# Kernel optimization log

Hardware: AMD Instinct MI355X
Metric: run time of the kernel (lower is better)

Reference implementation:

```python
import jax, jax.numpy as jnp
import numpy as np

B, S, D, H = 2, 2048, 1024, 16
HD = D // H
SCALE = HD ** -0.5


def setup_inputs() -> dict:
    key = jax.random.key(0)
    ks = jax.random.split(key, 9)
    w = 0.02
    return {
        "query": jax.random.normal(ks[0], (B, S, D), jnp.float32),
        "key": jax.random.normal(ks[1], (B, S, D), jnp.float32),
        "value": jax.random.normal(ks[2], (B, S, D), jnp.float32),
        # precomputed structural bias matrix B_struct [B, S, S]
        "bias_struct": jax.random.uniform(ks[3], (B, S, S), jnp.float32, 0.0, 1.5),
        "Wq": jax.random.normal(ks[4], (D, D), jnp.float32) * w,
        "bq": jnp.zeros((D,), jnp.float32),
        "Wk": jax.random.normal(ks[5], (D, D), jnp.float32) * w,
        "bk": jnp.zeros((D,), jnp.float32),
        "Wv": jax.random.normal(ks[6], (D, D), jnp.float32) * w,
        "bv": jnp.zeros((D,), jnp.float32),
        "Wo": jax.random.normal(ks[7], (D, D), jnp.float32) * w,
        "bo": jnp.zeros((D,), jnp.float32),
        "lambda_bias": jnp.array(1.0, jnp.float32),
    }


def _split_heads(x):
    # [B, S, D] -> [B, H, S, HD]
    b, s, _ = x.shape
    return x.reshape(b, s, H, HD).transpose(0, 2, 1, 3)


def reference(query, key, value, bias_struct, Wq, bq, Wk, bk, Wv, bv, Wo, bo, lambda_bias):
    # Linear projections (torch Linear: x @ W.T + b)
    Q = _split_heads(query @ Wq.T + bq)
    K = _split_heads(key @ Wk.T + bk)
    V = _split_heads(value @ Wv.T + bv)
    # scores = QK^T * scale + lambda * B_struct (broadcast over heads)
    scores = jnp.einsum("bhqd,bhkd->bhqk", Q, K) * SCALE
    scores = scores + lambda_bias * bias_struct[:, None, :, :]
    attn = jax.nn.softmax(scores, axis=-1)
    out = jnp.einsum("bhqk,bhkd->bhqd", attn, V)
    out = out.transpose(0, 2, 1, 3).reshape(query.shape[0], query.shape[1], D)
    return out @ Wo.T + bo
```

## Files before the change

### kernel.cpp

```cpp
#include <hip/hip_runtime.h>
#include <hip/hip_bf16.h>

namespace {

constexpr int B  = 2;
constexpr int S  = 2048;
constexpr int D  = 1024;
constexpr int H  = 16;
constexpr int BH = B * H;
constexpr float SCALE = 0.125f;
constexpr float LOG2E = 1.44269504f;
constexpr float SL2   = SCALE * LOG2E;
constexpr float THR2  = 8.0f * LOG2E;

constexpr int GM = B * S;
constexpr int GN = D;
constexpr int GK = D;

typedef __bf16 bf16x8 __attribute__((ext_vector_type(8)));
typedef float  f32x4  __attribute__((ext_vector_type(4)));
typedef unsigned short u16;
typedef u16 u16x8 __attribute__((ext_vector_type(8)));
typedef u16 u16x4 __attribute__((ext_vector_type(4)));

__device__ __forceinline__ u16 f2bf(float f) {
  union { float f; unsigned u; } v{f};
  unsigned r = v.u + 0x7fffu + ((v.u >> 16) & 1u);
  return (u16)(r >> 16);
}
__device__ __forceinline__ float bf2f(u16 u) {
  union { unsigned u; float f; } v{(unsigned)u << 16};
  return v.f;
}

__device__ __forceinline__ f32x4 mfma16(bf16x8 a, bf16x8 b, f32x4 c) {
  return __builtin_amdgcn_mfma_f32_16x16x32_bf16(a, b, c, 0, 0, 0);
}

__device__ __forceinline__ void gload_lds16(const u16* g, u16* l) {
  __builtin_amdgcn_global_load_lds(
      (const __attribute__((address_space(1))) void*)g,
      (__attribute__((address_space(3))) void*)l, 16, 0, 0);
}

__global__ __launch_bounds__(256) void cvt3_k(
    const float* __restrict__ a, const float* __restrict__ b,
    const float* __restrict__ c, u16* __restrict__ da,
    u16* __restrict__ db, u16* __restrict__ dc)
{
  const float* s = (blockIdx.z == 0) ? a : (blockIdx.z == 1) ? b : c;
  u16* d = (blockIdx.z == 0) ? da : (blockIdx.z == 1) ? db : dc;
  size_t i = ((size_t)blockIdx.x * 256 + threadIdx.x) * 4;
  float4 v = *(const float4*)&s[i];
  u16x4 o = { f2bf(v.x), f2bf(v.y), f2bf(v.z), f2bf(v.w) };
  *(u16x4*)&d[i] = o;
}

__global__ __launch_bounds__(256) void cvt4_k(
    const float* __restrict__ a, const float* __restrict__ b,
    const float* __restrict__ c, const float* __restrict__ e,
    u16* __restrict__ da, u16* __restrict__ db,
    u16* __restrict__ dc, u16* __restrict__ de)
{
  const float* s = (blockIdx.z == 0) ? a : (blockIdx.z == 1) ? b
                 : (blockIdx.z == 2) ? c : e;
  u16* d = (blockIdx.z == 0) ? da : (blockIdx.z == 1) ? db
         : (blockIdx.z == 2) ? dc : de;
  size_t i = ((size_t)blockIdx.x * 256 + threadIdx.x) * 4;
  float4 v = *(const float4*)&s[i];
  u16x4 o = { f2bf(v.x), f2bf(v.y), f2bf(v.z), f2bf(v.w) };
  *(u16x4*)&d[i] = o;
}

template <bool OUTBF, int NZ>
__global__ __launch_bounds__(256) void gemm_k(
    const u16* __restrict__ A0, const u16* __restrict__ A1, const u16* __restrict__ A2,
    const u16* __restrict__ W0, const u16* __restrict__ W1, const u16* __restrict__ W2,
    const float* __restrict__ b0, const float* __restrict__ b1, const float* __restrict__ b2,
    u16* __restrict__ C0, u16* __restrict__ C1, u16* __restrict__ C2,
    float* __restrict__ Cf)
{
  constexpr int BM = 128, BN = 64, BK = 64;
  __shared__ u16 Al[2][BM * BK];
  __shared__ u16 Bl[2][BN * BK];

  const int z = (NZ > 1) ? blockIdx.z : 0;
  const u16* Ap = (z == 0) ? A0 : (z == 1) ? A1 : A2;
  const u16* Wp = (z == 0) ? W0 : (z == 1) ? W1 : W2;
  const float* bias = (z == 0) ? b0 : (z == 1) ? b1 : b2;
  u16* Cb = (z == 0) ? C0 : (z == 1) ? C1 : C2;

  const int tid  = threadIdx.x;
  const int lane = tid & 63;
  const int w    = tid >> 6;
  const int wr = w >> 1, wc = w & 1;
  const int lg = lane >> 4, ll = lane & 15;
  const int bm = blockIdx.y * BM, bn = blockIdx.x * BN;

  auto STAGE = [&](int buf, int k0) {
#pragma unroll
    for (int i = 0; i < 4; ++i) {
      const int c = i * 256 + tid;
      const int row = c >> 3, cs = c & 7;
      const int dofs = ((cs * 16) ^ ((row & 7) << 4)) >> 1;
      gload_lds16(&Ap[(size_t)(bm + row) * GK + k0 + dofs], &Al[buf][c * 8]);
    }
#pragma unroll
    for (int i = 0; i < 2; ++i) {
      const int c = i * 256 + tid;
      const int row = c >> 3, cs = c & 7;
      const int dofs = ((cs * 16) ^ ((row & 7) << 4)) >> 1;
      gload_lds16(&Wp[(size_t)(bn + row) * GK + k0 + dofs], &Bl[buf][c * 8]);
    }
  };

  f32x4 acc[4][2] = {};

  STAGE(0, 0);
  __syncthreads();

  int cur = 0;
  constexpr int NT = GK / BK;
  for (int t = 0; t < NT; ++t) {
    if (t + 1 < NT) STAGE(cur ^ 1, (t + 1) * BK);
#pragma unroll
    for (int half = 0; half < 2; ++half) {
      bf16x8 af[4], bfr[2];
#pragma unroll
      for (int mi = 0; mi < 4; ++mi) {
        const int row = wr * 64 + mi * 16 + ll;
        af[mi] = *(const bf16x8*)&Al[cur][row * 64 +
                   (((half * 64 + lg * 16) ^ ((row & 7) << 4)) >> 1)];
      }
#pragma unroll
      for (int ni = 0; ni < 2; ++ni) {
        const int row = wc * 32 + ni * 16 + ll;
        bfr[ni] = *(const bf16x8*)&Bl[cur][row * 64 +
                   (((half * 64 + lg * 16) ^ ((row & 7) << 4)) >> 1)];
      }
#pragma unroll
      for (int mi = 0; mi < 4; ++mi)
#pragma unroll
        for (int ni = 0; ni < 2; ++ni)
          acc[mi][ni] = mfma16(af[mi], bfr[ni], acc[mi][ni]);
    }
    __syncthreads();
    cur ^= 1;
  }

#pragma unroll
  for (int ni = 0; ni < 2; ++ni) {
    const int gcol = bn + wc * 32 + ni * 16 + ll;
    const float bv = bias[gcol];
#pragma unroll
    for (int mi = 0; mi < 4; ++mi) {
      const int grow = bm + wr * 64 + mi * 16 + lg * 4;
#pragma unroll
      for (int r = 0; r < 4; ++r) {
        float v = acc[mi][ni][r] + bv;
        if (OUTBF) Cb[(size_t)(grow + r) * GN + gcol] = f2bf(v);
        else       Cf[(size_t)(grow + r) * GN + gcol] = v;
      }
    }
  }
}

__global__ __launch_bounds__(256) void transpose_v_k(
    const u16* __restrict__ Vb, u16* __restrict__ Vt)
{
  __shared__ u16 T[64][72];
  const int tid = threadIdx.x;
  const int bh = blockIdx.y, b = bh >> 4, h = bh & 15;
  const int s0 = blockIdx.x * 64;
#pragma unroll
  for (int it = 0; it < 2; ++it) {
    int idx = tid + it * 256;
    int s = idx >> 3, dc = idx & 7;
    *(uint4*)&T[s][dc * 8] =
        *(const uint4*)&Vb[(size_t)(b * S + s0 + s) * D + h * 64 + dc * 8];
  }
  __syncthreads();
#pragma unroll
  for (int it = 0; it < 2; ++it) {
    int idx = tid + it * 256;
    int d = idx >> 3, sc = idx & 7;
    u16x8 o;
#pragma unroll
    for (int jj = 0; jj < 8; ++jj) o[jj] = T[sc * 8 + jj][d];
    *(u16x8*)&Vt[((size_t)bh * 64 + d) * S + s0 + sc * 8] = o;
  }
}

__global__ __launch_bounds__(256) void attn_split_k(
    const u16* __restrict__ Qb, const u16* __restrict__ Kb,
    const u16* __restrict__ Vt, const float* __restrict__ biasS,
    const float* __restrict__ lamp, u16* __restrict__ Opart,
    float2* __restrict__ Ml)
{
  __shared__ u16 Kl[2][64 * 64];
  __shared__ __bf16 Pl[4][16][72];

  const int tid  = threadIdx.x;
  const int lane = tid & 63;
  const int w    = tid >> 6;
  const int lg = lane >> 4, ll = lane & 15;
  const int bh = blockIdx.y, b = bh >> 4, h = bh & 15;
  const int qw = blockIdx.x * 64 + w * 16;
  const int split = blockIdx.z;
  const int kvbase = split * (S / 2);
  const float lamS = lamp[0] * 8.0f;

  bf16x8 aQ[2];
  {
    const u16* qrow = &Qb[(size_t)(b * S + qw + ll) * D + h * 64];
    aQ[0] = *(const bf16x8*)&qrow[lg * 8];
    aQ[1] = *(const bf16x8*)&qrow[32 + lg * 8];
  }

  const u16* Kbase = &Kb[(size_t)(b * S + kvbase) * D + h * 64];
  const u16* Vbase = &Vt[(size_t)bh * 64 * S + kvbase];
  const float* Bb  = &biasS[((size_t)b * S + qw + lg * 4) * S + kvbase];

  auto STAGE_K = [&](int buf, int k0) {
#pragma unroll
    for (int i = 0; i < 2; ++i) {
      const int c   = (w * 2 + i) * 64 + lane;
      const int row = c >> 3, cs = c & 7;
      const int dofs = ((cs * 16) ^ ((row & 7) << 4)) >> 1;
      gload_lds16(&Kbase[(size_t)(k0 + row) * D + dofs],
                  &Kl[buf][(w * 2 + i) * 512]);
    }
  };

  f32x4 accO[4] = {};
  float m_r[4], l_r[4];
#pragma unroll
  for (int r = 0; r < 4; ++r) { m_r[r] = -1e30f; l_r[r] = 0.f; }

  STAGE_K(0, 0);
  __syncthreads();

  int cur = 0;
  constexpr int NT = (S / 2) / 64;
  for (int t = 0; t < NT; ++t) {
    const int k0 = t * 64;
    if (t + 1 < NT) STAGE_K(cur ^ 1, k0 + 64);

    f32x4 sf[4];
#pragma unroll
    for (int kf = 0; kf < 4; ++kf) {
      const int row = kf * 16 + ll;
      const u16* kr = &Kl[cur][row * 64];
      bf16x8 kb0 = *(const bf16x8*)&kr[((lg * 16) ^ ((row & 7) << 4)) >> 1];
      bf16x8 kb1 = *(const bf16x8*)&kr[((64 + lg * 16) ^ ((row & 7) << 4)) >> 1];
      f32x4 t4;
#pragma unroll
      for (int r = 0; r < 4; ++r)
        t4[r] = lamS * Bb[(size_t)r * S + k0 + kf * 16 + ll];
      t4 = mfma16(aQ[0], kb0, t4);
      t4 = mfma16(aQ[1], kb1, t4);
#pragma unroll
      for (int r = 0; r < 4; ++r) t4[r] *= SL2;
      sf[kf] = t4;
    }

    float pm[4];
#pragma unroll
    for (int r = 0; r < 4; ++r)
      pm[r] = fmaxf(fmaxf(sf[0][r], sf[1][r]), fmaxf(sf[2][r], sf[3][r]));
    float ex = fmaxf(fmaxf(pm[0] - m_r[0], pm[1] - m_r[1]),
                     fmaxf(pm[2] - m_r[2], pm[3] - m_r[3]));
    if (__any(ex > THR2)) {
#pragma unroll
      for (int r = 0; r < 4; ++r) {
        float tmx = pm[r];
        tmx = fmaxf(tmx, __shfl_xor(tmx, 1));
        tmx = fmaxf(tmx, __shfl_xor(tmx, 2));
        tmx = fmaxf(tmx, __shfl_xor(tmx, 4));
        tmx = fmaxf(tmx, __shfl_xor(tmx, 8));
        float nm = fmaxf(m_r[r], tmx);
        float cf = exp2f(m_r[r] - nm);
        m_r[r] = nm;
        l_r[r] *= cf;
#pragma unroll
        for (int nf = 0; nf < 4; ++nf) accO[nf][r] *= cf;
      }
    }
#pragma unroll
    for (int r = 0; r < 4; ++r) {
      float ps = 0.f;
#pragma unroll
      for (int kf = 0; kf < 4; ++kf) {
        float p = exp2f(sf[kf][r] - m_r[r]);
        Pl[w][lg * 4 + r][kf * 16 + ll] = (__bf16)p;
        ps += p;
      }
      l_r[r] += ps;
    }

    bf16x8 aP0 = *(const bf16x8*)&Pl[w][ll][lg * 8];
    bf16x8 aP1 = *(const bf16x8*)&Pl[w][ll][32 + lg * 8];
#pragma unroll
    for (int nf = 0; nf < 4; ++nf) {
      const u16* vrow = &Vbase[(size_t)(nf * 16 + ll) * S + k0];
      bf16x8 v0 = *(const bf16x8*)&vrow[lg * 8];
      bf16x8 v1 = *(const bf16x8*)&vrow[32 + lg * 8];
      accO[nf] = mfma16(aP0, v0, accO[nf]);
      accO[nf] = mfma16(aP1, v1, accO[nf]);
    }

    __syncthreads();
    cur ^= 1;
  }

#pragma unroll
  for (int r = 0; r < 4; ++r) {
    float tl = l_r[r];
    tl += __shfl_xor(tl, 1);
    tl += __shfl_xor(tl, 2);
    tl += __shfl_xor(tl, 4);
    tl += __shfl_xor(tl, 8);
    l_r[r] = tl;
  }

  u16* Op = Opart + (size_t)split * ((size_t)BH * S * 64);
  float2* Mlp = Ml + (size_t)split * ((size_t)BH * S);
  if (ll == 0) {
#pragma unroll
    for (int r = 0; r < 4; ++r) {
      float2 v; v.x = m_r[r]; v.y = l_r[r];
      Mlp[(size_t)bh * S + qw + lg * 4 + r] = v;
    }
  }
#pragma unroll
  for (int nf = 0; nf < 4; ++nf)
#pragma unroll
    for (int r = 0; r < 4; ++r)
      Op[((size_t)bh * S + qw + lg * 4 + r) * 64 + nf * 16 + ll] =
          f2bf(accO[nf][r]);
}

__global__ __launch_bounds__(256) void merge_k(
    const u16* __restrict__ Opart, const float2* __restrict__ Ml,
    u16* __restrict__ Obf)
{
  const int tid = threadIdx.x;
  const size_t row = (size_t)blockIdx.x * 32 + (tid >> 3);
  const int dc = (tid & 7) * 8;
  const float2 ml0 = Ml[row];
  const float2 ml1 = Ml[(size_t)BH * S + row];
  const float m = fmaxf(ml0.x, ml1.x);
  float c0 = exp2f(ml0.x - m), c1 = exp2f(ml1.x - m);
  const float inv = 1.0f / (c0 * ml0.y + c1 * ml1.y);
  c0 *= inv; c1 *= inv;
  u16x8 a = *(const u16x8*)&Opart[row * 64 + dc];
  u16x8 bq = *(const u16x8*)&Opart[(size_t)BH * S * 64 + row * 64 + dc];
  u16x8 o;
#pragma unroll
  for (int j = 0; j < 8; ++j)
    o[j] = f2bf(c0 * bf2f(a[j]) + c1 * bf2f(bq[j]));
  const int bh = (int)(row >> 11), q = (int)(row & 2047);
  *(u16x8*)&Obf[((size_t)((bh >> 4) * S + q)) * D + (bh & 15) * 64 + dc] = o;
}

}

extern "C" void kernel_launch(void* const* d_in, const int* in_sizes, int n_in,
                              void* d_out, int out_size, void* d_ws, size_t ws_size,
                              hipStream_t stream)
{
  const float* query = (const float*)d_in[0];
  const float* key   = (const float*)d_in[1];
  const float* value = (const float*)d_in[2];
  const float* biasS = (const float*)d_in[3];
  const float* Wq = (const float*)d_in[4];
  const float* bq = (const float*)d_in[5];
  const float* Wk = (const float*)d_in[6];
  const float* bk = (const float*)d_in[7];
  const float* Wv = (const float*)d_in[8];
  const float* bv = (const float*)d_in[9];
  const float* Wo = (const float*)d_in[10];
  const float* bo = (const float*)d_in[11];
  const float* lam = (const float*)d_in[12];
  float* out = (float*)d_out;

  char* ws = (char*)d_ws;
  const size_t MB = 1024 * 1024;
  u16* Xq  = (u16*)(ws + 0 * MB);
  u16* Xk  = (u16*)(ws + 8 * MB);
  u16* Xv  = (u16*)(ws + 16 * MB);
  u16* WqB = (u16*)(ws + 24 * MB);
  u16* WkB = (u16*)(ws + 26 * MB);
  u16* WvB = (u16*)(ws + 28 * MB);
  u16* WoB = (u16*)(ws + 30 * MB);
  u16* Qbf = (u16*)(ws + 32 * MB);
  u16* Kbf = (u16*)(ws + 40 * MB);
  u16* Opart = (u16*)ws;
  u16* Obf   = (u16*)(ws + 16 * MB);
  u16* Vbf = (u16*)d_out;
  u16* Vt  = (u16*)d_out + (size_t)4 * MB;
  float2* Ml = (float2*)d_out;

  cvt3_k<<<dim3(4096, 1, 3), 256, 0, stream>>>(query, key, value, Xq, Xk, Xv);
  cvt4_k<<<dim3(1024, 1, 4), 256, 0, stream>>>(Wq, Wk, Wv, Wo, WqB, WkB, WvB, WoB);

  dim3 pgrid(GN / 64, GM / 128, 3);
  gemm_k<true, 3><<<pgrid, 256, 0, stream>>>(
      Xq, Xk, Xv, WqB, WkB, WvB, bq, bk, bv, Qbf, Kbf, Vbf, nullptr);

  transpose_v_k<<<dim3(S / 64, B * H), 256, 0, stream>>>(Vbf, Vt);

  attn_split_k<<<dim3(S / 64, BH, 2), 256, 0, stream>>>(
      Qbf, Kbf, Vt, biasS, lam, Opart, Ml);

  merge_k<<<dim3(BH * S / 32), 256, 0, stream>>>(Opart, Ml, Obf);

  dim3 ogrid(GN / 64, GM / 128, 1);
  gemm_k<false, 1><<<ogrid, 256, 0, stream>>>(
      Obf, nullptr, nullptr, WoB, nullptr, nullptr, bo, nullptr, nullptr,
      nullptr, nullptr, nullptr, out);
}
```

Baseline: 387.6 us.

## Drop attention KV split and merge, retile GEMMs with k-major LDS layout

Attention goes back to one pass over all keys per query block, so the split-K partial buffers and the merge kernel are gone and output is normalized and written in place. The GEMMs become a templated kernel with BK=32, a k-group-major LDS layout without XOR swizzle, and larger 128x128 or 64x128 tiles. The softmax scale is folded into the Q projection epilogue, and the bias for the next tile is prefetched into registers. s_setprio is placed around MFMA blocks. The attention grid is halved, which may lower occupancy, and the unswizzled LDS layout may cause bank conflicts.

After: 448.5 us. 1.16x slower.

```diff
diff --git a/kernel.cpp b/kernel.cpp
--- a/kernel.cpp
+++ b/kernel.cpp
@@ -28,10 +28,6 @@
   unsigned r = v.u + 0x7fffu + ((v.u >> 16) & 1u);
   return (u16)(r >> 16);
 }
-__device__ __forceinline__ float bf2f(u16 u) {
-  union { unsigned u; float f; } v{(unsigned)u << 16};
-  return v.f;
-}
 
 __device__ __forceinline__ f32x4 mfma16(bf16x8 a, bf16x8 b, f32x4 c) {
   return __builtin_amdgcn_mfma_f32_16x16x32_bf16(a, b, c, 0, 0, 0);
@@ -72,19 +68,18 @@
   *(u16x4*)&d[i] = o;
 }
 
-template <bool OUTBF, int NZ>
-__global__ __launch_bounds__(256) void gemm_k(
+template <int BM, int BN, bool QKV>
+__global__ __launch_bounds__(256) void gemmT_k(
     const u16* __restrict__ A0, const u16* __restrict__ A1, const u16* __restrict__ A2,
     const u16* __restrict__ W0, const u16* __restrict__ W1, const u16* __restrict__ W2,
     const float* __restrict__ b0, const float* __restrict__ b1, const float* __restrict__ b2,
     u16* __restrict__ C0, u16* __restrict__ C1, u16* __restrict__ C2,
     float* __restrict__ Cf)
 {
-  constexpr int BM = 128, BN = 64, BK = 64;
-  __shared__ u16 Al[2][BM * BK];
-  __shared__ u16 Bl[2][BN * BK];
-
-  const int z = (NZ > 1) ? blockIdx.z : 0;
+  __shared__ u16 Al[2][4 * BM * 8];
+  __shared__ u16 Bl[2][4 * BN * 8];
+
+  const int z = QKV ? blockIdx.z : 0;
   const u16* Ap = (z == 0) ? A0 : (z == 1) ? A1 : A2;
   const u16* Wp = (z == 0) ? W0 : (z == 1) ? W1 : W2;
   const float* bias = (z == 0) ? b0 : (z == 1) ? b1 : b2;
@@ -99,67 +94,64 @@
 
   auto STAGE = [&](int buf, int k0) {
 #pragma unroll
-    for (int i = 0; i < 4; ++i) {
+    for (int i = 0; i < (4 * BM) / 256; ++i) {
       const int c = i * 256 + tid;
-      const int row = c >> 3, cs = c & 7;
-      const int dofs = ((cs * 16) ^ ((row & 7) << 4)) >> 1;
-      gload_lds16(&Ap[(size_t)(bm + row) * GK + k0 + dofs], &Al[buf][c * 8]);
-    }
-#pragma unroll
-    for (int i = 0; i < 2; ++i) {
+      const int kg = c / BM, row = c % BM;
+      gload_lds16(&Ap[(size_t)(bm + row) * GK + k0 + kg * 8], &Al[buf][c * 8]);
+    }
+#pragma unroll
+    for (int i = 0; i < (4 * BN) / 256; ++i) {
       const int c = i * 256 + tid;
-      const int row = c >> 3, cs = c & 7;
-      const int dofs = ((cs * 16) ^ ((row & 7) << 4)) >> 1;
-      gload_lds16(&Wp[(size_t)(bn + row) * GK + k0 + dofs], &Bl[buf][c * 8]);
+      const int kg = c / BN, row = c % BN;
+      gload_lds16(&Wp[(size_t)(bn + row) * GK + k0 + kg * 8], &Bl[buf][c * 8]);
     }
   };
 
-  f32x4 acc[4][2] = {};
+  constexpr int MI = BM / 32, NI = BN / 32;
+  f32x4 acc[MI][NI] = {};
 
   STAGE(0, 0);
   __syncthreads();
 
   int cur = 0;
-  constexpr int NT = GK / BK;
+  constexpr int NT = GK / 32;
   for (int t = 0; t < NT; ++t) {
-    if (t + 1 < NT) STAGE(cur ^ 1, (t + 1) * BK);
-#pragma unroll
-    for (int half = 0; half < 2; ++half) {
-      bf16x8 af[4], bfr[2];
-#pragma unroll
-      for (int mi = 0; mi < 4; ++mi) {
-        const int row = wr * 64 + mi * 16 + ll;
-        af[mi] = *(const bf16x8*)&Al[cur][row * 64 +
-                   (((half * 64 + lg * 16) ^ ((row & 7) << 4)) >> 1)];
-      }
-#pragma unroll
-      for (int ni = 0; ni < 2; ++ni) {
-        const int row = wc * 32 + ni * 16 + ll;
-        bfr[ni] = *(const bf16x8*)&Bl[cur][row * 64 +
-                   (((half * 64 + lg * 16) ^ ((row & 7) << 4)) >> 1)];
-      }
-#pragma unroll
-      for (int mi = 0; mi < 4; ++mi)
-#pragma unroll
-        for (int ni = 0; ni < 2; ++ni)
-          acc[mi][ni] = mfma16(af[mi], bfr[ni], acc[mi][ni]);
-    }
+    if (t + 1 < NT) STAGE(cur ^ 1, (t + 1) * 32);
+    bf16x8 af[MI], bfr[NI];
+#pragma unroll
+    for (int mi = 0; mi < MI; ++mi) {
+      const int arow = wr * (BM / 2) + mi * 16 + ll;
+      af[mi] = *(const bf16x8*)&Al[cur][(lg * BM + arow) * 8];
+    }
+#pragma unroll
+    for (int ni = 0; ni < NI; ++ni) {
+      const int brow = wc * (BN / 2) + ni * 16 + ll;
+      bfr[ni] = *(const bf16x8*)&Bl[cur][(lg * BN + brow) * 8];
+    }
+    __builtin_amdgcn_s_setprio(1);
+#pragma unroll
+    for (int mi = 0; mi < MI; ++mi)
+#pragma unroll
+      for (int ni = 0; ni < NI; ++ni)
+        acc[mi][ni] = mfma16(af[mi], bfr[ni], acc[mi][ni]);
+    __builtin_amdgcn_s_setprio(0);
     __syncthreads();
     cur ^= 1;
   }
 
-#pragma unroll
-  for (int ni = 0; ni < 2; ++ni) {
-    const int gcol = bn + wc * 32 + ni * 16 + ll;
+  const float sc = (QKV && z == 0) ? SL2 : 1.0f;
+#pragma unroll
+  for (int ni = 0; ni < NI; ++ni) {
+    const int gcol = bn + wc * (BN / 2) + ni * 16 + ll;
     const float bv = bias[gcol];
 #pragma unroll
-    for (int mi = 0; mi < 4; ++mi) {
-      const int grow = bm + wr * 64 + mi * 16 + lg * 4;
+    for (int mi = 0; mi < MI; ++mi) {
+      const int grow = bm + wr * (BM / 2) + mi * 16 + lg * 4;
 #pragma unroll
       for (int r = 0; r < 4; ++r) {
-        float v = acc[mi][ni][r] + bv;
-        if (OUTBF) Cb[(size_t)(grow + r) * GN + gcol] = f2bf(v);
-        else       Cf[(size_t)(grow + r) * GN + gcol] = v;
+        float v = (acc[mi][ni][r] + bv) * sc;
+        if (QKV) Cb[(size_t)(grow + r) * GN + gcol] = f2bf(v);
+        else     Cf[(size_t)(grow + r) * GN + gcol] = v;
       }
     }
   }
@@ -191,13 +183,12 @@
   }
 }
 
-__global__ __launch_bounds__(256) void attn_split_k(
+__global__ __launch_bounds__(256) void attn_k(
     const u16* __restrict__ Qb, const u16* __restrict__ Kb,
     const u16* __restrict__ Vt, const float* __restrict__ biasS,
-    const float* __restrict__ lamp, u16* __restrict__ Opart,
-    float2* __restrict__ Ml)
-{
-  __shared__ u16 Kl[2][64 * 64];
+    const float* __restrict__ lamp, u16* __restrict__ Ob)
+{
+  __shared__ u16 Kl[2][8 * 64 * 8];
   __shared__ __bf16 Pl[4][16][72];
 
   const int tid  = threadIdx.x;
@@ -206,9 +197,7 @@
   const int lg = lane >> 4, ll = lane & 15;
   const int bh = blockIdx.y, b = bh >> 4, h = bh & 15;
   const int qw = blockIdx.x * 64 + w * 16;
-  const int split = blockIdx.z;
-  const int kvbase = split * (S / 2);
-  const float lamS = lamp[0] * 8.0f;
+  const float lamL2 = lamp[0] * LOG2E;
 
   bf16x8 aQ[2];
   {
@@ -217,18 +206,16 @@
     aQ[1] = *(const bf16x8*)&qrow[32 + lg * 8];
   }
 
-  const u16* Kbase = &Kb[(size_t)(b * S + kvbase) * D + h * 64];
-  const u16* Vbase = &Vt[(size_t)bh * 64 * S + kvbase];
-  const float* Bb  = &biasS[((size_t)b * S + qw + lg * 4) * S + kvbase];
+  const u16* Kbase = &Kb[(size_t)(b * S) * D + h * 64];
+  const u16* Vbase = &Vt[(size_t)bh * 64 * S];
+  const float* Bb  = &biasS[((size_t)b * S + qw + lg * 4) * S];
 
   auto STAGE_K = [&](int buf, int k0) {
 #pragma unroll
     for (int i = 0; i < 2; ++i) {
-      const int c   = (w * 2 + i) * 64 + lane;
-      const int row = c >> 3, cs = c & 7;
-      const int dofs = ((cs * 16) ^ ((row & 7) << 4)) >> 1;
-      gload_lds16(&Kbase[(size_t)(k0 + row) * D + dofs],
-                  &Kl[buf][(w * 2 + i) * 512]);
+      const int c = i * 256 + tid;
+      const int kg = c >> 6, row = c & 63;
+      gload_lds16(&Kbase[(size_t)(k0 + row) * D + kg * 8], &Kl[buf][c * 8]);
     }
   };
 
@@ -237,11 +224,17 @@
 #pragma unroll
   for (int r = 0; r < 4; ++r) { m_r[r] = -1e30f; l_r[r] = 0.f; }
 
+  float bc[4][4];
   STAGE_K(0, 0);
+#pragma unroll
+  for (int r = 0; r < 4; ++r)
+#pragma unroll
+    for (int kf = 0; kf < 4; ++kf)
+      bc[r][kf] = lamL2 * Bb[(size_t)r * S + kf * 16 + ll];
   __syncthreads();
 
   int cur = 0;
-  constexpr int NT = (S / 2) / 64;
+  constexpr int NT = S / 64;
   for (int t = 0; t < NT; ++t) {
     const int k0 = t * 64;
     if (t + 1 < NT) STAGE_K(cur ^ 1, k0 + 64);
@@ -249,19 +242,22 @@
     f32x4 sf[4];
 #pragma unroll
     for (int kf = 0; kf < 4; ++kf) {
-      const int row = kf * 16 + ll;
-      const u16* kr = &Kl[cur][row * 64];
-      bf16x8 kb0 = *(const bf16x8*)&kr[((lg * 16) ^ ((row & 7) << 4)) >> 1];
-      bf16x8 kb1 = *(const bf16x8*)&kr[((64 + lg * 16) ^ ((row & 7) << 4)) >> 1];
-      f32x4 t4;
-#pragma unroll
-      for (int r = 0; r < 4; ++r)
-        t4[r] = lamS * Bb[(size_t)r * S + k0 + kf * 16 + ll];
+      bf16x8 kb0 = *(const bf16x8*)&Kl[cur][(lg * 64 + kf * 16 + ll) * 8];
+      bf16x8 kb1 = *(const bf16x8*)&Kl[cur][((4 + lg) * 64 + kf * 16 + ll) * 8];
+      f32x4 t4 = { bc[0][kf], bc[1][kf], bc[2][kf], bc[3][kf] };
+      __builtin_amdgcn_s_setprio(1);
       t4 = mfma16(aQ[0], kb0, t4);
       t4 = mfma16(aQ[1], kb1, t4);
-#pragma unroll
-      for (int r = 0; r < 4; ++r) t4[r] *= SL2;
+      __builtin_amdgcn_s_setprio(0);
       sf[kf] = t4;
+    }
+
+    if (t + 1 < NT) {
+#pragma unroll
+      for (int r = 0; r < 4; ++r)
+#pragma unroll
+        for (int kf = 0; kf < 4; ++kf)
+          bc[r][kf] = lamL2 * Bb[(size_t)r * S + k0 + 64 + kf * 16 + ll];
     }
 
     float pm[4];
@@ -305,14 +301,17 @@
       const u16* vrow = &Vbase[(size_t)(nf * 16 + ll) * S + k0];
       bf16x8 v0 = *(const bf16x8*)&vrow[lg * 8];
       bf16x8 v1 = *(const bf16x8*)&vrow[32 + lg * 8];
+      __builtin_amdgcn_s_setprio(1);
       accO[nf] = mfma16(aP0, v0, accO[nf]);
       accO[nf] = mfma16(aP1, v1, accO[nf]);
+      __builtin_amdgcn_s_setprio(0);
     }
 
     __syncthreads();
     cur ^= 1;
   }
 
+  float inv[4];
 #pragma unroll
   for (int r = 0; r < 4; ++r) {
     float tl = l_r[r];
@@ -320,47 +319,14 @@
     tl += __shfl_xor(tl, 2);
     tl += __shfl_xor(tl, 4);
     tl += __shfl_xor(tl, 8);
-    l_r[r] = tl;
-  }
-
-  u16* Op = Opart + (size_t)split * ((size_t)BH * S * 64);
-  float2* Mlp = Ml + (size_t)split * ((size_t)BH * S);
-  if (ll == 0) {
-#pragma unroll
-    for (int r = 0; r < 4; ++r) {
-      float2 v; v.x = m_r[r]; v.y = l_r[r];
-      Mlp[(size_t)bh * S + qw + lg * 4 + r] = v;
-    }
+    inv[r] = 1.0f / tl;
   }
 #pragma unroll
   for (int nf = 0; nf < 4; ++nf)
 #pragma unroll
     for (int r = 0; r < 4; ++r)
-      Op[((size_t)bh * S + qw + lg * 4 + r) * 64 + nf * 16 + ll] =
-          f2bf(accO[nf][r]);
-}
-
-__global__ __launch_bounds__(256) void merge_k(
-    const u16* __restrict__ Opart, const float2* __restrict__ Ml,
-    u16* __restrict__ Obf)
-{
-  const int tid = threadIdx.x;
-  const size_t row = (size_t)blockIdx.x * 32 + (tid >> 3);
-  const int dc = (tid & 7) * 8;
-  const float2 ml0 = Ml[row];
-  const float2 ml1 = Ml[(size_t)BH * S + row];
-  const float m = fmaxf(ml0.x, ml1.x);
-  float c0 = exp2f(ml0.x - m), c1 = exp2f(ml1.x - m);
-  const float inv = 1.0f / (c0 * ml0.y + c1 * ml1.y);
-  c0 *= inv; c1 *= inv;
-  u16x8 a = *(const u16x8*)&Opart[row * 64 + dc];
-  u16x8 bq = *(const u16x8*)&Opart[(size_t)BH * S * 64 + row * 64 + dc];
-  u16x8 o;
-#pragma unroll
-  for (int j = 0; j < 8; ++j)
-    o[j] = f2bf(c0 * bf2f(a[j]) + c1 * bf2f(bq[j]));
-  const int bh = (int)(row >> 11), q = (int)(row & 2047);
-  *(u16x8*)&Obf[((size_t)((bh >> 4) * S + q)) * D + (bh & 15) * 64 + dc] = o;
+      Ob[(size_t)(b * S + qw + lg * 4 + r) * D + h * 64 + nf * 16 + ll] =
+          f2bf(accO[nf][r] * inv[r]);
 }
 
 }
@@ -395,28 +361,23 @@
   u16* WoB = (u16*)(ws + 30 * MB);
   u16* Qbf = (u16*)(ws + 32 * MB);
   u16* Kbf = (u16*)(ws + 40 * MB);
-  u16* Opart = (u16*)ws;
-  u16* Obf   = (u16*)(ws + 16 * MB);
+  u16* Obf = Xq;
   u16* Vbf = (u16*)d_out;
   u16* Vt  = (u16*)d_out + (size_t)4 * MB;
-  float2* Ml = (float2*)d_out;
 
   cvt3_k<<<dim3(4096, 1, 3), 256, 0, stream>>>(query, key, value, Xq, Xk, Xv);
   cvt4_k<<<dim3(1024, 1, 4), 256, 0, stream>>>(Wq, Wk, Wv, Wo, WqB, WkB, WvB, WoB);
 
-  dim3 pgrid(GN / 64, GM / 128, 3);
-  gemm_k<true, 3><<<pgrid, 256, 0, stream>>>(
+  dim3 pgrid(GN / 128, GM / 128, 3);
+  gemmT_k<128, 128, true><<<pgrid, 256, 0, stream>>>(
       Xq, Xk, Xv, WqB, WkB, WvB, bq, bk, bv, Qbf, Kbf, Vbf, nullptr);
 
-  transpose_v_k<<<dim3(S / 64, B * H), 256, 0, stream>>>(Vbf, Vt);
-
-  attn_split_k<<<dim3(S / 64, BH, 2), 256, 0, stream>>>(
-      Qbf, Kbf, Vt, biasS, lam, Opart, Ml);
-
-  merge_k<<<dim3(BH * S / 32), 256, 0, stream>>>(Opart, Ml, Obf);
-
-  dim3 ogrid(GN / 64, GM / 128, 1);
-  gemm_k<false, 1><<<ogrid, 256, 0, stream>>>(
+  transpose_v_k<<<dim3(S / 64, BH), 256, 0, stream>>>(Vbf, Vt);
+
+  attn_k<<<dim3(S / 64, BH), 256, 0, stream>>>(Qbf, Kbf, Vt, biasS, lam, Obf);
+
+  dim3 ogrid(GN / 128, GM / 64, 1);
+  gemmT_k<64, 128, false><<<ogrid, 256, 0, stream>>>(
       Obf, nullptr, nullptr, WoB, nullptr, nullptr, bo, nullptr, nullptr,
       nullptr, nullptr, nullptr, out);
 }
```
